# Performance work log

Measured on AMD Instinct MI355X. Metric: run time of the kernel, lower is better.

Reference implementation:

```python
import jax, jax.numpy as jnp
import numpy as np

N_NODES = 4096
N_EDGES = 131072
IN_DIM = 40
HID = 128
OUT = 128
GAT_H = 2
GAT_C = 64
D_MODEL = 128
N_HEAD = 4
FF_DIM = 2048
N_LAYERS = 2
EPS = 1e-5
NEG_SLOPE = 0.2


def _layer_norm(x, g, b):
    mu = x.mean(-1, keepdims=True)
    var = ((x - mu) ** 2).mean(-1, keepdims=True)
    return (x - mu) / jnp.sqrt(var + EPS) * g + b


def _gat_conv(h, src, dst, W, a_src, a_dst, bias):
    # PyG GATConv, concat=True, eval mode (no dropout). Self loops already in (src, dst).
    N = h.shape[0]
    xw = (h @ W.T).reshape(N, GAT_H, GAT_C)          # [N, H, C]
    al_src = (xw * a_src).sum(-1)                     # [N, H]
    al_dst = (xw * a_dst).sum(-1)                     # [N, H]
    e = jax.nn.leaky_relu(al_src[src] + al_dst[dst], NEG_SLOPE)  # [E, H]
    # segment softmax over incoming edges of each dst node
    m = jax.ops.segment_max(e, dst, num_segments=N)
    ex = jnp.exp(e - m[dst])
    s = jax.ops.segment_sum(ex, dst, num_segments=N)
    alpha = ex / (s[dst] + 1e-16)                     # [E, H]
    out = jax.ops.segment_sum(xw[src] * alpha[..., None], dst, num_segments=N)
    return out.reshape(N, GAT_H * GAT_C) + bias


def _encoder_layer(x, p):
    # post-norm nn.TransformerEncoderLayer, relu FFN, eval mode
    (in_w, in_b, out_w, out_b, ln1_g, ln1_b,
     ff_w1, ff_b1, ff_w2, ff_b2, ln2_g, ln2_b) = p
    S, E = x.shape
    Dh = E // N_HEAD
    qkv = x @ in_w.T + in_b                           # [S, 3E]
    q, k, v = [t.reshape(S, N_HEAD, Dh) for t in jnp.split(qkv, 3, axis=-1)]
    scores = jnp.einsum('shd,thd->hst', q, k) / jnp.asarray(np.sqrt(Dh), x.dtype)
    attn = jax.nn.softmax(scores, axis=-1)            # [H, S, S]
    o = jnp.einsum('hst,thd->shd', attn, v).reshape(S, E) @ out_w.T + out_b
    x = _layer_norm(x + o, ln1_g, ln1_b)
    ff = jax.nn.relu(x @ ff_w1.T + ff_b1) @ ff_w2.T + ff_b2
    return _layer_norm(x + ff, ln2_g, ln2_b)


def _forward(floats, edge_index):
    (x, enc_w1, enc_b1, enc_w2, enc_b2,
     gat_w, gat_asrc, gat_adst, gat_b,
     l0_in_w, l0_in_b, l0_out_w, l0_out_b, l0_ln1_g, l0_ln1_b,
     l0_ff_w1, l0_ff_b1, l0_ff_w2, l0_ff_b2, l0_ln2_g, l0_ln2_b,
     l1_in_w, l1_in_b, l1_out_w, l1_out_b, l1_ln1_g, l1_ln1_b,
     l1_ff_w1, l1_ff_b1, l1_ff_w2, l1_ff_b2, l1_ln2_g, l1_ln2_b) = floats
    N = x.shape[0]
    # encoder MLP
    h = jax.nn.relu(x @ enc_w1.T + enc_b1) @ enc_w2.T + enc_b2
    # add one self loop per node (GATConv add_self_loops semantics)
    loop = jnp.arange(N, dtype=edge_index.dtype)
    src = jnp.concatenate([edge_index[0], loop])
    dst = jnp.concatenate([edge_index[1], loop])
    h = _gat_conv(h, src, dst, gat_w, gat_asrc, gat_adst, gat_b)
    layers = [
        (l0_in_w, l0_in_b, l0_out_w, l0_out_b, l0_ln1_g, l0_ln1_b,
         l0_ff_w1, l0_ff_b1, l0_ff_w2, l0_ff_b2, l0_ln2_g, l0_ln2_b),
        (l1_in_w, l1_in_b, l1_out_w, l1_out_b, l1_ln1_g, l1_ln1_b,
         l1_ff_w1, l1_ff_b1, l1_ff_w2, l1_ff_b2, l1_ln2_g, l1_ln2_b),
    ]
    for p in layers:
        h = _encoder_layer(h, p)
    return h


def setup_inputs() -> dict:
    key = jax.random.key(0)
    ks = jax.random.split(key, 40)
    s = 0.05
    inp = {}
    inp['x'] = jax.random.normal(ks[0], (N_NODES, IN_DIM), dtype=jnp.float32)
    # edges with src != dst (self loops added inside reference)
    src = jax.random.randint(ks[1], (N_EDGES,), 0, N_NODES)
    off = jax.random.randint(ks[2], (N_EDGES,), 1, N_NODES)
    dst = (src + off) % N_NODES
    inp['edge_index'] = jnp.stack([src, dst]).astype(jnp.int64)
    inp['enc_w1'] = jax.random.normal(ks[3], (HID, IN_DIM)) * s
    inp['enc_b1'] = jnp.zeros((HID,), jnp.float32)
    inp['enc_w2'] = jax.random.normal(ks[4], (OUT, HID)) * s
    inp['enc_b2'] = jnp.zeros((OUT,), jnp.float32)
    inp['gat_w'] = jax.random.normal(ks[5], (GAT_H * GAT_C, OUT)) * s
    inp['gat_asrc'] = jax.random.normal(ks[6], (GAT_H, GAT_C)) * s
    inp['gat_adst'] = jax.random.normal(ks[7], (GAT_H, GAT_C)) * s
    inp['gat_b'] = jnp.zeros((GAT_H * GAT_C,), jnp.float32)
    for i in range(N_LAYERS):
        k = jax.random.split(ks[8 + i], 8)
        inp[f'l{i}_in_w'] = jax.random.normal(k[0], (3 * D_MODEL, D_MODEL)) * s
        inp[f'l{i}_in_b'] = jnp.zeros((3 * D_MODEL,), jnp.float32)
        inp[f'l{i}_out_w'] = jax.random.normal(k[1], (D_MODEL, D_MODEL)) * s
        inp[f'l{i}_out_b'] = jnp.zeros((D_MODEL,), jnp.float32)
        inp[f'l{i}_ln1_g'] = jnp.ones((D_MODEL,), jnp.float32)
        inp[f'l{i}_ln1_b'] = jnp.zeros((D_MODEL,), jnp.float32)
        inp[f'l{i}_ff_w1'] = jax.random.normal(k[2], (FF_DIM, D_MODEL)) * s
        inp[f'l{i}_ff_b1'] = jnp.zeros((FF_DIM,), jnp.float32)
        inp[f'l{i}_ff_w2'] = jax.random.normal(k[3], (D_MODEL, FF_DIM)) * s
        inp[f'l{i}_ff_b2'] = jnp.zeros((D_MODEL,), jnp.float32)
        inp[f'l{i}_ln2_g'] = jnp.ones((D_MODEL,), jnp.float32)
        inp[f'l{i}_ln2_b'] = jnp.zeros((D_MODEL,), jnp.float32)
    return inp


def reference(x, edge_index, enc_w1, enc_b1, enc_w2, enc_b2,
              gat_w, gat_asrc, gat_adst, gat_b,
              l0_in_w, l0_in_b, l0_out_w, l0_out_b, l0_ln1_g, l0_ln1_b,
              l0_ff_w1, l0_ff_b1, l0_ff_w2, l0_ff_b2, l0_ln2_g, l0_ln2_b,
              l1_in_w, l1_in_b, l1_out_w, l1_out_b, l1_ln1_g, l1_ln1_b,
              l1_ff_w1, l1_ff_b1, l1_ff_w2, l1_ff_b2, l1_ln2_g, l1_ln2_b):
    floats = (x, enc_w1, enc_b1, enc_w2, enc_b2,
              gat_w, gat_asrc, gat_adst, gat_b,
              l0_in_w, l0_in_b, l0_out_w, l0_out_b, l0_ln1_g, l0_ln1_b,
              l0_ff_w1, l0_ff_b1, l0_ff_w2, l0_ff_b2, l0_ln2_g, l0_ln2_b,
              l1_in_w, l1_in_b, l1_out_w, l1_out_b, l1_ln1_g, l1_ln1_b,
              l1_ff_w1, l1_ff_b1, l1_ff_w2, l1_ff_b2, l1_ln2_g, l1_ln2_b)
    return _forward(floats, edge_index)
```

## Files before the change

### kernel.cpp

```cpp
#include <hip/hip_runtime.h>
#include <hip/hip_bf16.h>

typedef __hip_bfloat16 bf16;

#define N_NODES 4096
#define IN_DIM  40
#define DM      128
#define FF_DIM  2048
#define GAT_H   2
#define GAT_C   64
#define NHEAD   4
#define DH      32
#define LN_EPS  1e-5f
#define KSPLIT  8
#define FSPLIT  4

typedef short s8v __attribute__((ext_vector_type(8)));
typedef float f4v __attribute__((ext_vector_type(4)));

__device__ __forceinline__ float anyload(const void* p, size_t i, int isbf) {
    if (isbf) return __bfloat162float(((const bf16*)p)[i]);
    return ((const float*)p)[i];
}
__device__ __forceinline__ int geti(const int* ei, int i, int is64) {
    return is64 ? ei[2 * (size_t)i] : ei[i];
}
__device__ __forceinline__ ushort tob(float v) {
    bf16 b = __float2bfloat16(v);
    return *(ushort*)&b;
}

__global__ void probe_kernel(const void* ones_vec, const int* ei, int* flags,
                             int* __restrict__ deg) {
    int i = blockIdx.x * 256 + threadIdx.x;
    if (i < N_NODES) deg[i] = 0;
    if (i == 0) {
        unsigned u = ((const unsigned*)ones_vec)[0];
        flags[0] = (u == 0x3F803F80u) ? 1 : 0;
        const unsigned* e = (const unsigned*)ei;
        flags[1] = (e[1] == 0u && e[3] == 0u && e[5] == 0u && e[7] == 0u) ? 1 : 0;
    }
}

__global__ __launch_bounds__(256) void enc1_mfma_kernel(const void* __restrict__ X,
                                                        const void* __restrict__ W,
                                                        const void* __restrict__ bias,
                                                        ushort* __restrict__ Cb,
                                                        const int* __restrict__ flags) {
    const int isbf = flags[0];
    const int t = threadIdx.x;
    const int w = t >> 6, lane = t & 63;
    const int col = lane & 15, quad = lane >> 4;
    const int wr = (w & 1) * 16, wc = (w >> 1) * 32;
    const int row0 = blockIdx.y * 32, col0 = blockIdx.x * 64;
    __shared__ __align__(16) ushort As[32 * 72];
    __shared__ __align__(16) ushort Ws[64 * 72];
    {
        int r = t >> 3, c0 = (t & 7) * 8;
#pragma unroll
        for (int j = 0; j < 8; ++j) {
            int c = c0 + j;
            float v = (c < IN_DIM) ? anyload(X, (size_t)(row0 + r) * IN_DIM + c, isbf) : 0.f;
            As[r * 72 + c] = tob(v);
        }
    }
#pragma unroll
    for (int i = 0; i < 2; ++i) {
        int idx = t + i * 256;
        int r = idx >> 3, c0 = (idx & 7) * 8;
#pragma unroll
        for (int j = 0; j < 8; ++j) {
            int c = c0 + j;
            float v = (c < IN_DIM) ? anyload(W, (size_t)(col0 + r) * IN_DIM + c, isbf) : 0.f;
            Ws[r * 72 + c] = tob(v);
        }
    }
    __syncthreads();
    f4v zero = {0.f, 0.f, 0.f, 0.f};
    f4v acc[2] = {zero, zero};
    s8v a0  = *(const s8v*)&As[(wr + col) * 72 + quad * 8];
    s8v a1  = *(const s8v*)&As[(wr + col) * 72 + 32 + quad * 8];
    s8v b00 = *(const s8v*)&Ws[(wc + col) * 72 + quad * 8];
    s8v b10 = *(const s8v*)&Ws[(wc + 16 + col) * 72 + quad * 8];
    s8v b01 = *(const s8v*)&Ws[(wc + col) * 72 + 32 + quad * 8];
    s8v b11 = *(const s8v*)&Ws[(wc + 16 + col) * 72 + 32 + quad * 8];
    acc[0] = __builtin_amdgcn_mfma_f32_16x16x32_bf16(a0, b00, acc[0], 0, 0, 0);
    acc[1] = __builtin_amdgcn_mfma_f32_16x16x32_bf16(a0, b10, acc[1], 0, 0, 0);
    acc[0] = __builtin_amdgcn_mfma_f32_16x16x32_bf16(a1, b01, acc[0], 0, 0, 0);
    acc[1] = __builtin_amdgcn_mfma_f32_16x16x32_bf16(a1, b11, acc[1], 0, 0, 0);
#pragma unroll
    for (int nc = 0; nc < 2; ++nc) {
        int cc = col0 + wc + nc * 16 + col;
        float bv = anyload(bias, cc, isbf);
#pragma unroll
        for (int r = 0; r < 4; ++r) {
            int rr = row0 + wr + quad * 4 + r;
            float v = fmaxf(acc[nc][r] + bv, 0.f);
            Cb[(size_t)rr * DM + cc] = tob(v);
        }
    }
}

__global__ __launch_bounds__(256) void mfma_gemm_kernel(const ushort* __restrict__ A,
                                                        const void* __restrict__ W,
                                                        const void* __restrict__ bias,
                                                        float* __restrict__ Cf,
                                                        ushort* __restrict__ Cb,
                                                        ushort* __restrict__ vtb,
                                                        int M, int N, int K,
                                                        const int* __restrict__ flags,
                                                        int relu) {
    const int isbf = flags[0];
    const int t = threadIdx.x;
    const int w = t >> 6, lane = t & 63;
    const int col = lane & 15, quad = lane >> 4;
    const int wr = (w & 1) * 16, wc = (w >> 1) * 32;
    const int row0 = blockIdx.y * 32, col0 = blockIdx.x * 64;
    __shared__ __align__(16) ushort As[32 * 72];
    __shared__ __align__(16) ushort Ws[64 * 72];
    f4v zero = {0.f, 0.f, 0.f, 0.f};
    f4v acc[2] = {zero, zero};
    const int ar = t >> 3, ac = (t & 7) * 8;
    for (int k0 = 0; k0 < K; k0 += 64) {
        __syncthreads();
        *(uint4*)&As[ar * 72 + ac] = *(const uint4*)&A[(size_t)(row0 + ar) * K + k0 + ac];
        if (isbf) {
            const ushort* Wb = (const ushort*)W;
#pragma unroll
            for (int i = 0; i < 2; ++i) {
                int idx = t + i * 256;
                int r = idx >> 3, c = (idx & 7) * 8;
                *(uint4*)&Ws[r * 72 + c] = *(const uint4*)&Wb[(size_t)(col0 + r) * K + k0 + c];
            }
        } else {
            const float* Wf = (const float*)W;
#pragma unroll
            for (int i = 0; i < 2; ++i) {
                int idx = t + i * 256;
                int r = idx >> 3, c = (idx & 7) * 8;
#pragma unroll
                for (int j = 0; j < 8; ++j)
                    Ws[r * 72 + c + j] = tob(Wf[(size_t)(col0 + r) * K + k0 + c + j]);
            }
        }
        __syncthreads();
        s8v a0  = *(const s8v*)&As[(wr + col) * 72 + quad * 8];
        s8v a1  = *(const s8v*)&As[(wr + col) * 72 + 32 + quad * 8];
        s8v b00 = *(const s8v*)&Ws[(wc + col) * 72 + quad * 8];
        s8v b10 = *(const s8v*)&Ws[(wc + 16 + col) * 72 + quad * 8];
        s8v b01 = *(const s8v*)&Ws[(wc + col) * 72 + 32 + quad * 8];
        s8v b11 = *(const s8v*)&Ws[(wc + 16 + col) * 72 + 32 + quad * 8];
        acc[0] = __builtin_amdgcn_mfma_f32_16x16x32_bf16(a0, b00, acc[0], 0, 0, 0);
        acc[1] = __builtin_amdgcn_mfma_f32_16x16x32_bf16(a0, b10, acc[1], 0, 0, 0);
        acc[0] = __builtin_amdgcn_mfma_f32_16x16x32_bf16(a1, b01, acc[0], 0, 0, 0);
        acc[1] = __builtin_amdgcn_mfma_f32_16x16x32_bf16(a1, b11, acc[1], 0, 0, 0);
    }
#pragma unroll
    for (int nc = 0; nc < 2; ++nc) {
        int cc = col0 + wc + nc * 16 + col;
        float bv = bias ? anyload(bias, cc, isbf) : 0.f;
#pragma unroll
        for (int r = 0; r < 4; ++r) {
            int rr = row0 + wr + quad * 4 + r;
            float v = acc[nc][r] + bv;
            if (relu) v = fmaxf(v, 0.f);
            size_t off = (size_t)rr * N + cc;
            if (Cf) Cf[off] = v;
            if (Cb) Cb[off] = tob(v);
            if (vtb && cc >= 256) vtb[(size_t)(cc - 256) * N_NODES + rr] = tob(v);
        }
    }
}

__global__ __launch_bounds__(256) void mfma_gemm_splitk_kernel(const ushort* __restrict__ A,
                                                               const void* __restrict__ W,
                                                               float* __restrict__ Cpart,
                                                               int M, int N, int K, int kchunk,
                                                               const int* __restrict__ flags) {
    const int isbf = flags[0];
    const int t = threadIdx.x;
    const int w = t >> 6, lane = t & 63;
    const int col = lane & 15, quad = lane >> 4;
    const int wr = (w & 1) * 16, wc = (w >> 1) * 32;
    const int row0 = blockIdx.y * 32, col0 = blockIdx.x * 64;
    const int kz = blockIdx.z;
    const int k_beg = kz * kchunk, k_end = k_beg + kchunk;
    __shared__ __align__(16) ushort As[32 * 72];
    __shared__ __align__(16) ushort Ws[64 * 72];
    f4v zero = {0.f, 0.f, 0.f, 0.f};
    f4v acc[2] = {zero, zero};
    const int ar = t >> 3, ac = (t & 7) * 8;
    for (int k0 = k_beg; k0 < k_end; k0 += 64) {
        __syncthreads();
        *(uint4*)&As[ar * 72 + ac] = *(const uint4*)&A[(size_t)(row0 + ar) * K + k0 + ac];
        if (isbf) {
            const ushort* Wb = (const ushort*)W;
#pragma unroll
            for (int i = 0; i < 2; ++i) {
                int idx = t + i * 256;
                int r = idx >> 3, c = (idx & 7) * 8;
                *(uint4*)&Ws[r * 72 + c] = *(const uint4*)&Wb[(size_t)(col0 + r) * K + k0 + c];
            }
        } else {
            const float* Wf = (const float*)W;
#pragma unroll
            for (int i = 0; i < 2; ++i) {
                int idx = t + i * 256;
                int r = idx >> 3, c = (idx & 7) * 8;
#pragma unroll
                for (int j = 0; j < 8; ++j)
                    Ws[r * 72 + c + j] = tob(Wf[(size_t)(col0 + r) * K + k0 + c + j]);
            }
        }
        __syncthreads();
        s8v a0  = *(const s8v*)&As[(wr + col) * 72 + quad * 8];
        s8v a1  = *(const s8v*)&As[(wr + col) * 72 + 32 + quad * 8];
        s8v b00 = *(const s8v*)&Ws[(wc + col) * 72 + quad * 8];
        s8v b10 = *(const s8v*)&Ws[(wc + 16 + col) * 72 + quad * 8];
        s8v b01 = *(const s8v*)&Ws[(wc + col) * 72 + 32 + quad * 8];
        s8v b11 = *(const s8v*)&Ws[(wc + 16 + col) * 72 + 32 + quad * 8];
        acc[0] = __builtin_amdgcn_mfma_f32_16x16x32_bf16(a0, b00, acc[0], 0, 0, 0);
        acc[1] = __builtin_amdgcn_mfma_f32_16x16x32_bf16(a0, b10, acc[1], 0, 0, 0);
        acc[0] = __builtin_amdgcn_mfma_f32_16x16x32_bf16(a1, b01, acc[0], 0, 0, 0);
        acc[1] = __builtin_amdgcn_mfma_f32_16x16x32_bf16(a1, b11, acc[1], 0, 0, 0);
    }
#pragma unroll
    for (int nc = 0; nc < 2; ++nc) {
        int cc = col0 + wc + nc * 16 + col;
#pragma unroll
        for (int r = 0; r < 4; ++r) {
            int rr = row0 + wr + quad * 4 + r;
            Cpart[((size_t)kz * M + rr) * N + cc] = acc[nc][r];
        }
    }
}

__global__ void deg_hist_kernel(const int* __restrict__ ei, int E0,
                                int* __restrict__ deg, const int* __restrict__ flags) {
    const int is64 = flags[1];
    int e = blockIdx.x * 256 + threadIdx.x;
    int E = E0 + N_NODES;
    if (e >= E) return;
    int d = (e < E0) ? geti(ei, E0 + e, is64) : (e - E0);
    atomicAdd(&deg[d], 1);
}

__global__ __launch_bounds__(256) void scan_kernel(const int* __restrict__ deg,
                                                   int* __restrict__ rowptr,
                                                   int* __restrict__ cursor) {
    __shared__ int part[256];
    const int t = threadIdx.x;
    const int base = t * 16;
    int loc[16];
    int s = 0;
#pragma unroll
    for (int i = 0; i < 16; ++i) { loc[i] = s; s += deg[base + i]; }
    part[t] = s;
    __syncthreads();
    for (int d = 1; d < 256; d <<= 1) {
        int v = (t >= d) ? part[t - d] : 0;
        __syncthreads();
        part[t] += v;
        __syncthreads();
    }
    int prev = (t == 0) ? 0 : part[t - 1];
#pragma unroll
    for (int i = 0; i < 16; ++i) {
        int r = prev + loc[i];
        rowptr[base + i] = r;
        cursor[base + i] = r;
    }
    if (t == 255) rowptr[N_NODES] = part[255];
}

__global__ void scatter_kernel(const int* __restrict__ ei, int E0,
                               int* __restrict__ cursor, int* __restrict__ csr_src,
                               const int* __restrict__ flags) {
    const int is64 = flags[1];
    int e = blockIdx.x * 256 + threadIdx.x;
    int E = E0 + N_NODES;
    if (e >= E) return;
    int s = (e < E0) ? geti(ei, e, is64) : (e - E0);
    int d = (e < E0) ? geti(ei, E0 + e, is64) : (e - E0);
    int pos = atomicAdd(&cursor[d], 1);
    csr_src[pos] = s;
}

__global__ void gat_al_kernel(const float* __restrict__ xw,
                              const void* __restrict__ asrc,
                              const void* __restrict__ adst,
                              float* __restrict__ als, float* __restrict__ ald,
                              const int* __restrict__ flags) {
    const int isbf = flags[0];
    int i = blockIdx.x * 256 + threadIdx.x;
    if (i >= N_NODES * GAT_H) return;
    int n = i >> 1, h = i & 1;
    const float* xr = xw + (size_t)n * DM + h * GAT_C;
    float ss = 0.f, sd = 0.f;
#pragma unroll 4
    for (int c = 0; c < GAT_C; ++c) {
        float v = xr[c];
        ss += v * anyload(asrc, h * GAT_C + c, isbf);
        sd += v * anyload(adst, h * GAT_C + c, isbf);
    }
    als[i] = ss;
    ald[i] = sd;
}

__global__ __launch_bounds__(256) void gat_gather_kernel(const int* __restrict__ rowptr,
                                                         const int* __restrict__ csr_src,
                                                         const float* __restrict__ als,
                                                         const float* __restrict__ ald,
                                                         const float* __restrict__ xw,
                                                         const void* __restrict__ gat_b,
                                                         float* __restrict__ hg,
                                                         ushort* __restrict__ hgb,
                                                         const int* __restrict__ flags) {
    const int isbf = flags[0];
    const int idx = blockIdx.x * 4 + (threadIdx.x >> 6);
    const int lane = threadIdx.x & 63;
    const int d = idx >> 1, hh = idx & 1;
    const int beg = rowptr[d], end = rowptr[d + 1];
    const float aldv = ald[d * 2 + hh];

    float mx = -3.0e38f;
    for (int i = beg + lane; i < end; i += 64) {
        int s = csr_src[i];
        float v = als[s * 2 + hh] + aldv;
        v = (v > 0.f) ? v : 0.2f * v;
        mx = fmaxf(mx, v);
    }
#pragma unroll
    for (int o = 32; o >= 1; o >>= 1) mx = fmaxf(mx, __shfl_xor(mx, o));
    float sm = 0.f;
    for (int i = beg + lane; i < end; i += 64) {
        int s = csr_src[i];
        float v = als[s * 2 + hh] + aldv;
        v = (v > 0.f) ? v : 0.2f * v;
        sm += __expf(v - mx);
    }
#pragma unroll
    for (int o = 32; o >= 1; o >>= 1) sm += __shfl_xor(sm, o);
    const float inv = 1.f / (sm + 1e-16f);

    float o_acc = 0.f;
    for (int i = beg; i < end; ++i) {
        int s = csr_src[i];
        float v = als[s * 2 + hh] + aldv;
        v = (v > 0.f) ? v : 0.2f * v;
        float alpha = __expf(v - mx) * inv;
        o_acc += alpha * xw[(size_t)s * DM + hh * GAT_C + lane];
    }
    float outv = o_acc + anyload(gat_b, hh * GAT_C + lane, isbf);
    size_t off = (size_t)d * DM + hh * GAT_C + lane;
    hg[off] = outv;
    hgb[off] = tob(outv);
}

#define KSTR 40
#define VSTR 136
#define PSTR 136
__global__ __launch_bounds__(256) void attn_mfma_kernel(const ushort* __restrict__ qkvb,
                                                        const ushort* __restrict__ vtb,
                                                        float* __restrict__ pO,
                                                        float* __restrict__ pL) {
    const int hh = blockIdx.y;
    const int kz = blockIdx.z;
    const int t = threadIdx.x;
    const int w = t >> 6;
    const int lane = t & 63;
    const int col = lane & 15;
    const int quad = lane >> 4;
    const int qr = blockIdx.x * 64 + w * 16;

    __shared__ __align__(16) ushort Ks[128 * KSTR];
    __shared__ __align__(16) ushort Vt[32 * VSTR];
    __shared__ __align__(16) ushort Pl[4][16 * PSTR];

    s8v aq = *(const s8v*)&qkvb[(size_t)(qr + col) * 384 + hh * 32 + quad * 8];

    f4v zero = {0.f, 0.f, 0.f, 0.f};
    f4v of[2] = {zero, zero};
    float lacc[4] = {0.f, 0.f, 0.f, 0.f};
    const float scale = 0.17677669529663687f;
    const int k_beg = kz * (N_NODES / KSPLIT);
    const int k_end = k_beg + (N_NODES / KSPLIT);

    for (int kt = k_beg; kt < k_end; kt += 128) {
        __syncthreads();
        for (int idx = t; idx < 512; idx += 256) {
            int r = idx >> 2, c = (idx & 3) * 8;
            *(uint4*)&Ks[r * KSTR + c] =
                *(const uint4*)&qkvb[(size_t)(kt + r) * 384 + 128 + hh * 32 + c];
        }
        for (int idx = t; idx < 512; idx += 256) {
            int d = idx >> 4, c = (idx & 15) * 8;
            *(uint4*)&Vt[d * VSTR + c] =
                *(const uint4*)&vtb[(size_t)(hh * 32 + d) * N_NODES + kt + c];
        }
        __syncthreads();

        f4v sf[8];
#pragma unroll
        for (int kb = 0; kb < 8; ++kb) {
            s8v bk = *(const s8v*)&Ks[(kb * 16 + col) * KSTR + quad * 8];
            sf[kb] = __builtin_amdgcn_mfma_f32_16x16x32_bf16(aq, bk, zero, 0, 0, 0);
        }
#pragma unroll
        for (int kb = 0; kb < 8; ++kb) {
#pragma unroll
            for (int r = 0; r < 4; ++r) {
                float p = __expf(sf[kb][r] * scale);
                lacc[r] += p;
                Pl[w][(quad * 4 + r) * PSTR + kb * 16 + col] = tob(p);
            }
        }
#pragma unroll
        for (int kc = 0; kc < 4; ++kc) {
            s8v ap = *(const s8v*)&Pl[w][col * PSTR + kc * 32 + quad * 8];
#pragma unroll
            for (int nc = 0; nc < 2; ++nc) {
                s8v bv = *(const s8v*)&Vt[(nc * 16 + col) * VSTR + kc * 32 + quad * 8];
                of[nc] = __builtin_amdgcn_mfma_f32_16x16x32_bf16(ap, bv, of[nc], 0, 0, 0);
            }
        }
    }
#pragma unroll
    for (int r = 0; r < 4; ++r) {
        float lv = lacc[r];
#pragma unroll
        for (int off = 1; off <= 8; off <<= 1) lv += __shfl_xor(lv, off);
        int row = quad * 4 + r;
        size_t qi = ((size_t)kz * N_NODES + qr + row) * NHEAD + hh;
#pragma unroll
        for (int nc = 0; nc < 2; ++nc)
            pO[qi * 32 + nc * 16 + col] = of[nc][r];
        if (col == 0) pL[qi] = lv;
    }
}

__global__ __launch_bounds__(256) void attn_combine_kernel(const float* __restrict__ pO,
                                                           const float* __restrict__ pL,
                                                           ushort* __restrict__ attnb) {
    int i = blockIdx.x * 256 + threadIdx.x;
    int q = i >> 7;
    int hh = (i >> 5) & 3;
    int d = i & 31;
    size_t qi0 = (size_t)q * NHEAD + hh;
    float lsum = 0.f, osum = 0.f;
#pragma unroll
    for (int kz = 0; kz < KSPLIT; ++kz) {
        size_t qi = qi0 + (size_t)kz * N_NODES * NHEAD;
        lsum += pL[qi];
        osum += pO[qi * 32 + d];
    }
    attnb[(size_t)q * DM + hh * 32 + d] = tob(osum / lsum);
}

__global__ __launch_bounds__(256) void ln_kernel(float* __restrict__ h, const float* __restrict__ y,
                                                 ushort* __restrict__ hb,
                                                 const void* __restrict__ g, const void* __restrict__ b,
                                                 const int* __restrict__ flags) {
    const int isbf = flags[0];
    const int row = blockIdx.x * 4 + (threadIdx.x >> 6);
    const int lane = threadIdx.x & 63;
    const size_t base = (size_t)row * DM;
    float v0 = h[base + lane] + y[base + lane];
    float v1 = h[base + 64 + lane] + y[base + 64 + lane];
    float s = v0 + v1;
#pragma unroll
    for (int o = 32; o >= 1; o >>= 1) s += __shfl_xor(s, o);
    float mu = s * (1.f / DM);
    float d0 = v0 - mu, d1 = v1 - mu;
    float q = d0 * d0 + d1 * d1;
#pragma unroll
    for (int o = 32; o >= 1; o >>= 1) q += __shfl_xor(q, o);
    float rstd = rsqrtf(q * (1.f / DM) + LN_EPS);
    float o0 = d0 * rstd * anyload(g, lane, isbf) + anyload(b, lane, isbf);
    float o1 = d1 * rstd * anyload(g, 64 + lane, isbf) + anyload(b, 64 + lane, isbf);
    h[base + lane] = o0;       h[base + 64 + lane] = o1;
    hb[base + lane] = tob(o0); hb[base + 64 + lane] = tob(o1);
}

__global__ __launch_bounds__(256) void ln4_kernel(float* __restrict__ h,
                                                  const float* __restrict__ pC,
                                                  const void* __restrict__ fbias,
                                                  ushort* __restrict__ hb,
                                                  const void* __restrict__ g, const void* __restrict__ b,
                                                  const int* __restrict__ flags) {
    const int isbf = flags[0];
    const int row = blockIdx.x * 4 + (threadIdx.x >> 6);
    const int lane = threadIdx.x & 63;
    const size_t base = (size_t)row * DM;
    float y0 = anyload(fbias, lane, isbf), y1 = anyload(fbias, 64 + lane, isbf);
#pragma unroll
    for (int kz = 0; kz < FSPLIT; ++kz) {
        size_t pb = (size_t)kz * N_NODES * DM + base;
        y0 += pC[pb + lane];
        y1 += pC[pb + 64 + lane];
    }
    float v0 = h[base + lane] + y0;
    float v1 = h[base + 64 + lane] + y1;
    float s = v0 + v1;
#pragma unroll
    for (int o = 32; o >= 1; o >>= 1) s += __shfl_xor(s, o);
    float mu = s * (1.f / DM);
    float d0 = v0 - mu, d1 = v1 - mu;
    float q = d0 * d0 + d1 * d1;
#pragma unroll
    for (int o = 32; o >= 1; o >>= 1) q += __shfl_xor(q, o);
    float rstd = rsqrtf(q * (1.f / DM) + LN_EPS);
    float o0 = d0 * rstd * anyload(g, lane, isbf) + anyload(b, lane, isbf);
    float o1 = d1 * rstd * anyload(g, 64 + lane, isbf) + anyload(b, 64 + lane, isbf);
    h[base + lane] = o0;       h[base + 64 + lane] = o1;
    hb[base + lane] = tob(o0); hb[base + 64 + lane] = tob(o1);
}

__global__ void convert_out_kernel(const float* __restrict__ h, void* __restrict__ out, int n,
                                   const int* __restrict__ flags) {
    const int isbf = flags[0];
    int i = blockIdx.x * 256 + threadIdx.x;
    if (i < n) {
        if (isbf) ((ushort*)out)[i] = tob(h[i]);
        else      ((float*)out)[i] = h[i];
    }
}

extern "C" void kernel_launch(void* const* d_in, const int* in_sizes, int n_in,
                              void* d_out, int out_size, void* d_ws, size_t ws_size,
                              hipStream_t stream) {
    const void* x        = d_in[0];
    const int*  ei       = (const int*)d_in[1];
    const void* enc_w1   = d_in[2];
    const void* enc_b1   = d_in[3];
    const void* enc_w2   = d_in[4];
    const void* enc_b2   = d_in[5];
    const void* gat_w    = d_in[6];
    const void* gat_asrc = d_in[7];
    const void* gat_adst = d_in[8];
    const void* gat_b    = d_in[9];
    const void *in_w[2], *in_b[2], *out_w[2], *out_b[2], *ln1_g[2], *ln1_b[2];
    const void *ff_w1[2], *ff_b1[2], *ff_w2[2], *ff_b2[2], *ln2_g[2], *ln2_b[2];
    for (int L = 0; L < 2; ++L) {
        int base = 10 + L * 12;
        in_w[L]  = d_in[base + 0];
        in_b[L]  = d_in[base + 1];
        out_w[L] = d_in[base + 2];
        out_b[L] = d_in[base + 3];
        ln1_g[L] = d_in[base + 4];
        ln1_b[L] = d_in[base + 5];
        ff_w1[L] = d_in[base + 6];
        ff_b1[L] = d_in[base + 7];
        ff_w2[L] = d_in[base + 8];
        ff_b2[L] = d_in[base + 9];
        ln2_g[L] = d_in[base + 10];
        ln2_b[L] = d_in[base + 11];
    }
    const int E0 = in_sizes[1] / 2;
    const int E  = E0 + N_NODES;
    const size_t NN = N_NODES;

    int*    flags   = (int*)d_ws;
    float*  h       = (float*)d_ws + 64;
    float*  tmp     = h + NN * DM;
    ushort* hb      = (ushort*)(tmp + NN * DM);
    ushort* attnb   = hb + NN * DM;
    ushort* hid     = attnb;
    ushort* qkvb    = attnb + NN * DM;
    ushort* vtb     = qkvb + NN * 384;
    float*  pO      = (float*)(vtb + NN * DM);
    float*  pL      = pO + (size_t)KSPLIT * NN * NHEAD * 32;
    float*  pC      = pL + (size_t)KSPLIT * NN * NHEAD;
    ushort* ff1b    = (ushort*)(pC + (size_t)FSPLIT * NN * DM);
    float*  xw      = (float*)(ff1b + NN * FF_DIM);
    float*  als     = xw + NN * DM;
    float*  ald     = als + NN * GAT_H;
    int*    deg     = (int*)(ald + NN * GAT_H);
    int*    rowptr  = deg + N_NODES;
    int*    cursor  = rowptr + N_NODES + 1;
    int*    csr_src = cursor + N_NODES;

    dim3 blk(256);

    probe_kernel<<<dim3(16), blk, 0, stream>>>(ln1_g[0], ei, flags, deg);
    deg_hist_kernel<<<dim3((E + 255) / 256), blk, 0, stream>>>(ei, E0, deg, flags);
    scan_kernel<<<dim3(1), blk, 0, stream>>>(deg, rowptr, cursor);
    scatter_kernel<<<dim3((E + 255) / 256), blk, 0, stream>>>(ei, E0, cursor, csr_src, flags);

    enc1_mfma_kernel<<<dim3(DM / 64, N_NODES / 32), blk, 0, stream>>>(
        x, enc_w1, enc_b1, hid, flags);
    mfma_gemm_kernel<<<dim3(DM / 64, N_NODES / 32), blk, 0, stream>>>(
        hid, enc_w2, enc_b2, nullptr, hb, nullptr, N_NODES, DM, DM, flags, 0);

    mfma_gemm_kernel<<<dim3(DM / 64, N_NODES / 32), blk, 0, stream>>>(
        hb, gat_w, nullptr, xw, nullptr, nullptr, N_NODES, DM, DM, flags, 0);
    gat_al_kernel<<<dim3((N_NODES * GAT_H + 255) / 256), blk, 0, stream>>>(
        xw, gat_asrc, gat_adst, als, ald, flags);
    gat_gather_kernel<<<dim3(N_NODES * GAT_H / 4), blk, 0, stream>>>(
        rowptr, csr_src, als, ald, xw, gat_b, h, hb, flags);

    for (int L = 0; L < 2; ++L) {
        mfma_gemm_kernel<<<dim3(3 * DM / 64, N_NODES / 32), blk, 0, stream>>>(
            hb, in_w[L], in_b[L], nullptr, qkvb, vtb, N_NODES, 3 * DM, DM, flags, 0);
        attn_mfma_kernel<<<dim3(N_NODES / 64, NHEAD, KSPLIT), blk, 0, stream>>>(
            qkvb, vtb, pO, pL);
        attn_combine_kernel<<<dim3(N_NODES * NHEAD * 32 / 256), blk, 0, stream>>>(
            pO, pL, attnb);
        mfma_gemm_kernel<<<dim3(DM / 64, N_NODES / 32), blk, 0, stream>>>(
            attnb, out_w[L], out_b[L], tmp, nullptr, nullptr, N_NODES, DM, DM, flags, 0);
        ln_kernel<<<dim3(N_NODES / 4), blk, 0, stream>>>(h, tmp, hb, ln1_g[L], ln1_b[L], flags);
        mfma_gemm_kernel<<<dim3(FF_DIM / 64, N_NODES / 32), blk, 0, stream>>>(
            hb, ff_w1[L], ff_b1[L], nullptr, ff1b, nullptr, N_NODES, FF_DIM, DM, flags, 1);
        mfma_gemm_splitk_kernel<<<dim3(DM / 64, N_NODES / 32, FSPLIT), blk, 0, stream>>>(
            ff1b, ff_w2[L], pC, N_NODES, DM, FF_DIM, FF_DIM / FSPLIT, flags);
        ln4_kernel<<<dim3(N_NODES / 4), blk, 0, stream>>>(h, pC, ff_b2[L], hb, ln2_g[L], ln2_b[L], flags);
    }

    convert_out_kernel<<<dim3((out_size + 255) / 256), blk, 0, stream>>>(h, d_out, out_size, flags);
}
```

Before: 358.4 us.

## Specialize K=128 GEMM and fuse attention split-K combine into out-projection

Replaces the generic looped GEMM with a K=128 kernel that loads the whole K extent into shared memory once, using 16-row tiles where each wave computes one 16x16 output tile. The out-projection GEMM now reduces the split-K attention partials (pO/pL) directly while building its A tile, which removes the separate attn_combine kernel and its intermediate buffer round trip. In exchange, the reduction over pO is done redundantly by each column block of the out-projection, and smaller row tiles mean the weight tiles are reloaded more often.

```diff
diff --git a/kernel.cpp b/kernel.cpp
--- a/kernel.cpp
+++ b/kernel.cpp
@@ -101,74 +101,90 @@
     }
 }
 
-__global__ __launch_bounds__(256) void mfma_gemm_kernel(const ushort* __restrict__ A,
+#define K128STR 136
+__global__ __launch_bounds__(256) void k128_gemm_kernel(const ushort* __restrict__ A,
+                                                        const float* __restrict__ pO,
+                                                        const float* __restrict__ pL,
                                                         const void* __restrict__ W,
                                                         const void* __restrict__ bias,
                                                         float* __restrict__ Cf,
                                                         ushort* __restrict__ Cb,
                                                         ushort* __restrict__ vtb,
-                                                        int M, int N, int K,
+                                                        int N,
                                                         const int* __restrict__ flags,
                                                         int relu) {
     const int isbf = flags[0];
     const int t = threadIdx.x;
     const int w = t >> 6, lane = t & 63;
     const int col = lane & 15, quad = lane >> 4;
-    const int wr = (w & 1) * 16, wc = (w >> 1) * 32;
-    const int row0 = blockIdx.y * 32, col0 = blockIdx.x * 64;
-    __shared__ __align__(16) ushort As[32 * 72];
-    __shared__ __align__(16) ushort Ws[64 * 72];
-    f4v zero = {0.f, 0.f, 0.f, 0.f};
-    f4v acc[2] = {zero, zero};
-    const int ar = t >> 3, ac = (t & 7) * 8;
-    for (int k0 = 0; k0 < K; k0 += 64) {
-        __syncthreads();
-        *(uint4*)&As[ar * 72 + ac] = *(const uint4*)&A[(size_t)(row0 + ar) * K + k0 + ac];
-        if (isbf) {
-            const ushort* Wb = (const ushort*)W;
-#pragma unroll
-            for (int i = 0; i < 2; ++i) {
-                int idx = t + i * 256;
-                int r = idx >> 3, c = (idx & 7) * 8;
-                *(uint4*)&Ws[r * 72 + c] = *(const uint4*)&Wb[(size_t)(col0 + r) * K + k0 + c];
+    const int wc = w * 16;
+    const int row0 = blockIdx.y * 16, col0 = blockIdx.x * 64;
+    __shared__ __align__(16) ushort As[16 * K128STR];
+    __shared__ __align__(16) ushort Ws[64 * K128STR];
+
+    {
+        int ar = t >> 4, ac = (t & 15) * 8;
+        if (pO) {
+            int rr = row0 + ar;
+            int hh = ac >> 5, d0 = ac & 31;
+            size_t qi0 = ((size_t)rr) * NHEAD + hh;
+            float lsum = 0.f;
+            float osum[8] = {};
+#pragma unroll
+            for (int kz = 0; kz < KSPLIT; ++kz) {
+                size_t qi = qi0 + (size_t)kz * N_NODES * NHEAD;
+                lsum += pL[qi];
+                const float* po = &pO[qi * 32 + d0];
+#pragma unroll
+                for (int j = 0; j < 8; ++j) osum[j] += po[j];
             }
+            float inv = 1.f / lsum;
+#pragma unroll
+            for (int j = 0; j < 8; ++j) As[ar * K128STR + ac + j] = tob(osum[j] * inv);
         } else {
-            const float* Wf = (const float*)W;
-#pragma unroll
-            for (int i = 0; i < 2; ++i) {
-                int idx = t + i * 256;
-                int r = idx >> 3, c = (idx & 7) * 8;
-#pragma unroll
-                for (int j = 0; j < 8; ++j)
-                    Ws[r * 72 + c + j] = tob(Wf[(size_t)(col0 + r) * K + k0 + c + j]);
-            }
-        }
-        __syncthreads();
-        s8v a0  = *(const s8v*)&As[(wr + col) * 72 + quad * 8];
-        s8v a1  = *(const s8v*)&As[(wr + col) * 72 + 32 + quad * 8];
-        s8v b00 = *(const s8v*)&Ws[(wc + col) * 72 + quad * 8];
-        s8v b10 = *(const s8v*)&Ws[(wc + 16 + col) * 72 + quad * 8];
-        s8v b01 = *(const s8v*)&Ws[(wc + col) * 72 + 32 + quad * 8];
-        s8v b11 = *(const s8v*)&Ws[(wc + 16 + col) * 72 + 32 + quad * 8];
-        acc[0] = __builtin_amdgcn_mfma_f32_16x16x32_bf16(a0, b00, acc[0], 0, 0, 0);
-        acc[1] = __builtin_amdgcn_mfma_f32_16x16x32_bf16(a0, b10, acc[1], 0, 0, 0);
-        acc[0] = __builtin_amdgcn_mfma_f32_16x16x32_bf16(a1, b01, acc[0], 0, 0, 0);
-        acc[1] = __builtin_amdgcn_mfma_f32_16x16x32_bf16(a1, b11, acc[1], 0, 0, 0);
-    }
-#pragma unroll
-    for (int nc = 0; nc < 2; ++nc) {
-        int cc = col0 + wc + nc * 16 + col;
-        float bv = bias ? anyload(bias, cc, isbf) : 0.f;
-#pragma unroll
-        for (int r = 0; r < 4; ++r) {
-            int rr = row0 + wr + quad * 4 + r;
-            float v = acc[nc][r] + bv;
-            if (relu) v = fmaxf(v, 0.f);
-            size_t off = (size_t)rr * N + cc;
-            if (Cf) Cf[off] = v;
-            if (Cb) Cb[off] = tob(v);
-            if (vtb && cc >= 256) vtb[(size_t)(cc - 256) * N_NODES + rr] = tob(v);
-        }
+            *(uint4*)&As[ar * K128STR + ac] = *(const uint4*)&A[(size_t)(row0 + ar) * DM + ac];
+        }
+    }
+    if (isbf) {
+        const ushort* Wb = (const ushort*)W;
+#pragma unroll
+        for (int i = 0; i < 4; ++i) {
+            int idx = t + i * 256;
+            int r = idx >> 4, c = (idx & 15) * 8;
+            *(uint4*)&Ws[r * K128STR + c] = *(const uint4*)&Wb[(size_t)(col0 + r) * DM + c];
+        }
+    } else {
+        const float* Wf = (const float*)W;
+#pragma unroll
+        for (int i = 0; i < 4; ++i) {
+            int idx = t + i * 256;
+            int r = idx >> 4, c = (idx & 15) * 8;
+#pragma unroll
+            for (int j = 0; j < 8; ++j)
+                Ws[r * K128STR + c + j] = tob(Wf[(size_t)(col0 + r) * DM + c + j]);
+        }
+    }
+    __syncthreads();
+
+    f4v acc = {0.f, 0.f, 0.f, 0.f};
+#pragma unroll
+    for (int j = 0; j < 4; ++j) {
+        s8v a = *(const s8v*)&As[col * K128STR + j * 32 + quad * 8];
+        s8v b = *(const s8v*)&Ws[(wc + col) * K128STR + j * 32 + quad * 8];
+        acc = __builtin_amdgcn_mfma_f32_16x16x32_bf16(a, b, acc, 0, 0, 0);
+    }
+
+    int cc = col0 + wc + col;
+    float bv = bias ? anyload(bias, cc, isbf) : 0.f;
+#pragma unroll
+    for (int r = 0; r < 4; ++r) {
+        int rr = row0 + quad * 4 + r;
+        float v = acc[r] + bv;
+        if (relu) v = fmaxf(v, 0.f);
+        size_t off = (size_t)rr * N + cc;
+        if (Cf) Cf[off] = v;
+        if (Cb) Cb[off] = tob(v);
+        if (vtb && cc >= 256) vtb[(size_t)(cc - 256) * N_NODES + rr] = tob(v);
     }
 }
 
@@ -437,24 +453,6 @@
             pO[qi * 32 + nc * 16 + col] = of[nc][r];
         if (col == 0) pL[qi] = lv;
     }
-}
-
-__global__ __launch_bounds__(256) void attn_combine_kernel(const float* __restrict__ pO,
-                                                           const float* __restrict__ pL,
-                                                           ushort* __restrict__ attnb) {
-    int i = blockIdx.x * 256 + threadIdx.x;
-    int q = i >> 7;
-    int hh = (i >> 5) & 3;
-    int d = i & 31;
-    size_t qi0 = (size_t)q * NHEAD + hh;
-    float lsum = 0.f, osum = 0.f;
-#pragma unroll
-    for (int kz = 0; kz < KSPLIT; ++kz) {
-        size_t qi = qi0 + (size_t)kz * N_NODES * NHEAD;
-        lsum += pL[qi];
-        osum += pO[qi * 32 + d];
-    }
-    attnb[(size_t)q * DM + hh * 32 + d] = tob(osum / lsum);
 }
 
 __global__ __launch_bounds__(256) void ln_kernel(float* __restrict__ h, const float* __restrict__ y,
@@ -564,9 +562,8 @@
     float*  h       = (float*)d_ws + 64;
     float*  tmp     = h + NN * DM;
     ushort* hb      = (ushort*)(tmp + NN * DM);
-    ushort* attnb   = hb + NN * DM;
-    ushort* hid     = attnb;
-    ushort* qkvb    = attnb + NN * DM;
+    ushort* hid     = hb + NN * DM;
+    ushort* qkvb    = hid + NN * DM;
     ushort* vtb     = qkvb + NN * 384;
     float*  pO      = (float*)(vtb + NN * DM);
     float*  pL      = pO + (size_t)KSPLIT * NN * NHEAD * 32;
@@ -589,28 +586,26 @@
 
     enc1_mfma_kernel<<<dim3(DM / 64, N_NODES / 32), blk, 0, stream>>>(
         x, enc_w1, enc_b1, hid, flags);
-    mfma_gemm_kernel<<<dim3(DM / 64, N_NODES / 32), blk, 0, stream>>>(
-        hid, enc_w2, enc_b2, nullptr, hb, nullptr, N_NODES, DM, DM, flags, 0);
-
-    mfma_gemm_kernel<<<dim3(DM / 64, N_NODES / 32), blk, 0, stream>>>(
-        hb, gat_w, nullptr, xw, nullptr, nullptr, N_NODES, DM, DM, flags, 0);
+    k128_gemm_kernel<<<dim3(DM / 64, N_NODES / 16), blk, 0, stream>>>(
+        hid, nullptr, nullptr, enc_w2, enc_b2, nullptr, hb, nullptr, DM, flags, 0);
+
+    k128_gemm_kernel<<<dim3(DM / 64, N_NODES / 16), blk, 0, stream>>>(
+        hb, nullptr, nullptr, gat_w, nullptr, xw, nullptr, nullptr, DM, flags, 0);
     gat_al_kernel<<<dim3((N_NODES * GAT_H + 255) / 256), blk, 0, stream>>>(
         xw, gat_asrc, gat_adst, als, ald, flags);
     gat_gather_kernel<<<dim3(N_NODES * GAT_H / 4), blk, 0, stream>>>(
         rowptr, csr_src, als, ald, xw, gat_b, h, hb, flags);
 
     for (int L = 0; L < 2; ++L) {
-        mfma_gemm_kernel<<<dim3(3 * DM / 64, N_NODES / 32), blk, 0, stream>>>(
-            hb, in_w[L], in_b[L], nullptr, qkvb, vtb, N_NODES, 3 * DM, DM, flags, 0);
+        k128_gemm_kernel<<<dim3(3 * DM / 64, N_NODES / 16), blk, 0, stream>>>(
+            hb, nullptr, nullptr, in_w[L], in_b[L], nullptr, qkvb, vtb, 3 * DM, flags, 0);
         attn_mfma_kernel<<<dim3(N_NODES / 64, NHEAD, KSPLIT), blk, 0, stream>>>(
             qkvb, vtb, pO, pL);
-        attn_combine_kernel<<<dim3(N_NODES * NHEAD * 32 / 256), blk, 0, stream>>>(
-            pO, pL, attnb);
-        mfma_gemm_kernel<<<dim3(DM / 64, N_NODES / 32), blk, 0, stream>>>(
-            attnb, out_w[L], out_b[L], tmp, nullptr, nullptr, N_NODES, DM, DM, flags, 0);
+        k128_gemm_kernel<<<dim3(DM / 64, N_NODES / 16), blk, 0, stream>>>(
+            nullptr, pO, pL, out_w[L], out_b[L], tmp, nullptr, nullptr, DM, flags, 0);
         ln_kernel<<<dim3(N_NODES / 4), blk, 0, stream>>>(h, tmp, hb, ln1_g[L], ln1_b[L], flags);
-        mfma_gemm_kernel<<<dim3(FF_DIM / 64, N_NODES / 32), blk, 0, stream>>>(
-            hb, ff_w1[L], ff_b1[L], nullptr, ff1b, nullptr, N_NODES, FF_DIM, DM, flags, 1);
+        k128_gemm_kernel<<<dim3(FF_DIM / 64, N_NODES / 16), blk, 0, stream>>>(
+            hb, nullptr, nullptr, ff_w1[L], ff_b1[L], nullptr, ff1b, nullptr, FF_DIM, flags, 1);
         mfma_gemm_splitk_kernel<<<dim3(DM / 64, N_NODES / 32, FSPLIT), blk, 0, stream>>>(
             ff1b, ff_w2[L], pC, N_NODES, DM, FF_DIM, FF_DIM / FSPLIT, flags);
         ln4_kernel<<<dim3(N_NODES / 4), blk, 0, stream>>>(h, pC, ff_b2[L], hb, ln2_g[L], ln2_b[L], flags);
```

Result: no change. 357.3 us (-0.3%).
